# Performance work log

Measured on AMD Instinct MI355X. Metric: run time of the kernel, lower is better.

The kernel has to match this reference:

```python
import jax, jax.numpy as jnp
import numpy as np

N, M, F, NBR = 100000, 12, 64, 64
EPS = 1e-5


def setup_inputs() -> dict:
    key = jax.random.key(0)
    ks = jax.random.split(key, 6)
    atom_in_fea = jax.random.normal(ks[0], (N, F), dtype=jnp.float32)
    nbr_fea = jax.random.normal(ks[1], (N, M, NBR), dtype=jnp.float32)
    bond_weights = jax.random.uniform(ks[2], (N, M), dtype=jnp.float32)
    nbr_fea_idx = jax.random.randint(ks[3], (N, M), 0, N)
    W = jax.random.normal(ks[4], (2 * F, 2 * F + NBR), dtype=jnp.float32) * 0.05
    b = jnp.zeros((2 * F,), dtype=jnp.float32)
    gamma1 = jnp.ones((2 * F,), dtype=jnp.float32)
    beta1 = jnp.zeros((2 * F,), dtype=jnp.float32)
    gamma2 = jnp.ones((F,), dtype=jnp.float32)
    beta2 = jnp.zeros((F,), dtype=jnp.float32)
    return dict(atom_in_fea=atom_in_fea, nbr_fea=nbr_fea, bond_weights=bond_weights,
                nbr_fea_idx=nbr_fea_idx, W=W, b=b, gamma1=gamma1, beta1=beta1,
                gamma2=gamma2, beta2=beta2)


def _batchnorm(x, gamma, beta):
    # training-mode BN over axis 0 with biased variance (torch BatchNorm1d)
    mean = x.mean(axis=0)
    var = ((x - mean) ** 2).mean(axis=0)
    return (x - mean) * jax.lax.rsqrt(var + EPS) * gamma + beta


def reference(atom_in_fea, nbr_fea, bond_weights, nbr_fea_idx, W, b,
              gamma1, beta1, gamma2, beta2):
    n, m = nbr_fea_idx.shape
    f = atom_in_fea.shape[1]
    atom_nbr_fea = atom_in_fea[nbr_fea_idx]                      # (N, M, F) gather
    self_fea = jnp.broadcast_to(atom_in_fea[:, None, :], (n, m, f))
    total = jnp.concatenate([self_fea, atom_nbr_fea, nbr_fea], axis=2)  # (N, M, 2F+NBR)
    gated = jnp.einsum('nmk,ok->nmo', total, W) + b              # (N, M, 2F)
    gated = _batchnorm(gated.reshape(-1, 2 * f), gamma1, beta1).reshape(n, m, 2 * f)
    nbr_filter = jax.nn.sigmoid(gated[..., :f]) * bond_weights[..., None]
    nbr_core = jax.nn.softplus(gated[..., f:]) * bond_weights[..., None]
    nbr_sumed = jnp.sum(nbr_filter * nbr_core, axis=1)           # (N, F)
    nbr_sumed = _batchnorm(nbr_sumed, gamma2, beta2)
    return jax.nn.softplus(atom_in_fea + nbr_sumed)
```

## Files before the change

kernel.cpp:

```cpp
#include <hip/hip_runtime.h>
#include <hip/hip_bf16.h>

typedef unsigned short ushort_t;
typedef __attribute__((ext_vector_type(8))) short bf16x8;
typedef __attribute__((ext_vector_type(4))) float f32x4;

#define NATOM 100000
#define NM    12
#define FD    64
#define KD    192
#define OD    128
#define NGRP  6250
#define ROWS1 1200000.0f
#define EPSBN 1e-5f


__device__ __forceinline__ float bf2f(ushort_t u) {
    unsigned int x = ((unsigned int)u) << 16;
    float f; __builtin_memcpy(&f, &x, 4); return f;
}
__device__ __forceinline__ ushort_t f2b(float f) {
    unsigned int x; __builtin_memcpy(&x, &f, 4);
    x += 0x7FFFu + ((x >> 16) & 1u);
    return (ushort_t)(x >> 16);
}

template<int DT>
__device__ __forceinline__ float ld1(const void* p, long i) {
    if constexpr (DT == 1) return bf2f(((const ushort_t*)p)[i]);
    else                   return ((const float*)p)[i];
}
template<int DT>
__device__ __forceinline__ void st1(void* p, long i, float v) {
    if constexpr (DT == 1) ((ushort_t*)p)[i] = f2b(v);
    else                   ((float*)p)[i] = v;
}
template<int DT>
__device__ __forceinline__ bf16x8 ld8(const void* p, long i) {
    if constexpr (DT == 1) {
        return *(const bf16x8*)((const ushort_t*)p + i);
    } else {
        const float4* f = (const float4*)((const float*)p + i);
        float4 a = f[0], b = f[1];
        bf16x8 r;
        r[0] = (short)f2b(a.x); r[1] = (short)f2b(a.y);
        r[2] = (short)f2b(a.z); r[3] = (short)f2b(a.w);
        r[4] = (short)f2b(b.x); r[5] = (short)f2b(b.y);
        r[6] = (short)f2b(b.z); r[7] = (short)f2b(b.w);
        return r;
    }
}

__global__ void k0_flag(const unsigned int* __restrict__ g1w, int* __restrict__ flag) {
    if (threadIdx.x == 0 && blockIdx.x == 0)
        *flag = (g1w[0] == 0x3F800000u) ? 0 : 1;
}

template<int DT>
__device__ __forceinline__ void stage_W(bf16x8* Wlds, const void* Wg, int tid) {
    for (int c = tid; c < 3072; c += 256) {
        int g = c >> 6, l = c & 63;
        int t = g / 6, s = g % 6;
        int row = t * 16 + (l & 15);
        int col = s * 32 + (l >> 4) * 8;
        Wlds[c] = ld8<DT>(Wg, row * KD + col);
    }
}

template<int DT>
__global__ __launch_bounds__(256) void k1_stats(
    const void* __restrict__ atomg, const void* __restrict__ nbrg,
    const int* __restrict__ idxg, const void* __restrict__ Wg,
    const int* __restrict__ flag, float* __restrict__ s1sum, float* __restrict__ s1sq)
{
    if (*flag != DT) return;
    __shared__ __align__(16) bf16x8 Wlds[3072];
    const int tid = threadIdx.x;
    const int w = tid >> 6, lane = tid & 63, la = lane & 15, q = lane >> 4;

    stage_W<DT>(Wlds, Wg, tid);
    __syncthreads();

    float sum[8], sq[8];
#pragma unroll
    for (int t = 0; t < 8; ++t) { sum[t] = 0.f; sq[t] = 0.f; }

    for (int grp = blockIdx.x; grp < NGRP; grp += gridDim.x) {
        const int n0 = grp << 4;
        const long selfo = (long)(n0 + la) * FD + q * 8;
        for (int it = 0; it < 3; ++it) {
            const int m = it * 4 + w;
            const int nb = idxg[(n0 + la) * NM + m];

            bf16x8 af[6];
            af[0] = ld8<DT>(atomg, selfo);
            af[1] = ld8<DT>(atomg, selfo + 32);
            af[2] = ld8<DT>(atomg, (long)nb * FD + q * 8);
            af[3] = ld8<DT>(atomg, (long)nb * FD + q * 8 + 32);
            af[4] = ld8<DT>(nbrg, ((long)(n0 + la) * NM + m) * FD + q * 8);
            af[5] = ld8<DT>(nbrg, ((long)(n0 + la) * NM + m) * FD + q * 8 + 32);

            f32x4 acc[8];
#pragma unroll
            for (int t = 0; t < 8; ++t) acc[t] = (f32x4){0.f, 0.f, 0.f, 0.f};
#pragma unroll
            for (int s = 0; s < 6; ++s) {
#pragma unroll
                for (int t = 0; t < 8; ++t) {
                    bf16x8 bfr = Wlds[(t * 6 + s) * 64 + lane];
                    acc[t] = __builtin_amdgcn_mfma_f32_16x16x32_bf16(af[s], bfr, acc[t], 0, 0, 0);
                }
            }
#pragma unroll
            for (int t = 0; t < 8; ++t)
#pragma unroll
                for (int r = 0; r < 4; ++r) {
                    float v = acc[t][r];
                    sum[t] += v; sq[t] += v * v;
                }
        }
    }

    const int rep = blockIdx.x & 7;
#pragma unroll
    for (int t = 0; t < 8; ++t) {
        float s = sum[t], z = sq[t];
        s += __shfl_xor(s, 16); s += __shfl_xor(s, 32);
        z += __shfl_xor(z, 16); z += __shfl_xor(z, 32);
        if (lane < 16) {
            atomicAdd(&s1sum[rep * OD + t * 16 + lane], s);
            atomicAdd(&s1sq [rep * OD + t * 16 + lane], z);
        }
    }
}

template<int DT>
__global__ __launch_bounds__(256) void k2_main(
    const void* __restrict__ atomg, const void* __restrict__ nbrg,
    const void* __restrict__ bwg, const int* __restrict__ idxg,
    const void* __restrict__ Wg,
    const void* __restrict__ g1p, const void* __restrict__ b1p,
    const float* __restrict__ s1sum, const float* __restrict__ s1sq,
    const int* __restrict__ flag,
    void* __restrict__ nsum, float* __restrict__ s2sum, float* __restrict__ s2sq)
{
    if (*flag != DT) return;
    __shared__ __align__(16) bf16x8 Wlds[3072];
    __shared__ float pred[4][16][64];
    const int tid = threadIdx.x;
    const int w = tid >> 6, lane = tid & 63, la = lane & 15, q = lane >> 4;

    stage_W<DT>(Wlds, Wg, tid);

    float scale[8], shift[8];
#pragma unroll
    for (int t = 0; t < 8; ++t) {
        int o = t * 16 + la;
        float sm = 0.f, sv = 0.f;
#pragma unroll
        for (int r = 0; r < 8; ++r) { sm += s1sum[r * OD + o]; sv += s1sq[r * OD + o]; }
        float mean = sm / ROWS1;
        float var  = sv / ROWS1 - mean * mean;
        float inv  = 1.0f / sqrtf(var + EPSBN);
        float ga   = ld1<DT>(g1p, o) * inv;
        scale[t] = ga;
        shift[t] = ld1<DT>(b1p, o) - mean * ga;
    }
    __syncthreads();

    float bsum = 0.f, bsq = 0.f;

    for (int grp = blockIdx.x; grp < NGRP; grp += gridDim.x) {
        const int n0 = grp << 4;
        const long selfo = (long)(n0 + la) * FD + q * 8;
        float psum[4][4];
#pragma unroll
        for (int t = 0; t < 4; ++t)
#pragma unroll
            for (int r = 0; r < 4; ++r) psum[t][r] = 0.f;

        for (int it = 0; it < 3; ++it) {
            const int m = it * 4 + w;
            const int nb = idxg[(n0 + la) * NM + m];

            bf16x8 af[6];
            af[0] = ld8<DT>(atomg, selfo);
            af[1] = ld8<DT>(atomg, selfo + 32);
            af[2] = ld8<DT>(atomg, (long)nb * FD + q * 8);
            af[3] = ld8<DT>(atomg, (long)nb * FD + q * 8 + 32);
            af[4] = ld8<DT>(nbrg, ((long)(n0 + la) * NM + m) * FD + q * 8);
            af[5] = ld8<DT>(nbrg, ((long)(n0 + la) * NM + m) * FD + q * 8 + 32);

            f32x4 acc[8];
#pragma unroll
            for (int t = 0; t < 8; ++t) acc[t] = (f32x4){0.f, 0.f, 0.f, 0.f};
#pragma unroll
            for (int s = 0; s < 6; ++s) {
#pragma unroll
                for (int t = 0; t < 8; ++t) {
                    bf16x8 bfr = Wlds[(t * 6 + s) * 64 + lane];
                    acc[t] = __builtin_amdgcn_mfma_f32_16x16x32_bf16(af[s], bfr, acc[t], 0, 0, 0);
                }
            }
#pragma unroll
            for (int r = 0; r < 4; ++r) {
                float bwv = ld1<DT>(bwg, (long)(n0 + q * 4 + r) * NM + m);
                float b2 = bwv * bwv;
#pragma unroll
                for (int t = 0; t < 4; ++t) {
                    float y1 = acc[t][r]     * scale[t]     + shift[t];
                    float y2 = acc[t + 4][r] * scale[t + 4] + shift[t + 4];
                    float sg = 1.0f / (1.0f + __expf(-y1));
                    float ax = fabsf(y2);
                    float sp = fmaxf(y2, 0.0f) + __logf(1.0f + __expf(-ax));
                    psum[t][r] += sg * sp * b2;
                }
            }
        }

#pragma unroll
        for (int t = 0; t < 4; ++t)
#pragma unroll
            for (int r = 0; r < 4; ++r)
                pred[w][q * 4 + r][t * 16 + la] = psum[t][r];
        __syncthreads();
        for (int e = tid; e < 1024; e += 256) {
            int a = e >> 6, c = e & 63;
            float v = pred[0][a][c] + pred[1][a][c] + pred[2][a][c] + pred[3][a][c];
            float vr;
            if constexpr (DT == 1) {
                ushort_t h = f2b(v);
                ((ushort_t*)nsum)[(long)(n0 + a) * FD + c] = h;
                vr = bf2f(h);
            } else {
                ((float*)nsum)[(long)(n0 + a) * FD + c] = v;
                vr = v;
            }
            bsum += vr; bsq += vr * vr;
        }
        __syncthreads();
    }

    const int rep = blockIdx.x & 7;
    atomicAdd(&s2sum[rep * FD + (tid & 63)], bsum);
    atomicAdd(&s2sq [rep * FD + (tid & 63)], bsq);
}

template<int DT>
__global__ __launch_bounds__(256) void k3_final(
    const void* __restrict__ atomg, void* __restrict__ nsum_out,
    const float* __restrict__ s2sum, const float* __restrict__ s2sq,
    const void* __restrict__ g2p, const void* __restrict__ b2p,
    const int* __restrict__ flag)
{
    if (*flag != DT) return;
    const int tid = blockIdx.x * 256 + threadIdx.x;
    const int c = tid & 63;
    float sm = 0.f, sv = 0.f;
#pragma unroll
    for (int r = 0; r < 8; ++r) { sm += s2sum[r * FD + c]; sv += s2sq[r * FD + c]; }
    float mean = sm / 100000.0f;
    float var  = sv / 100000.0f - mean * mean;
    float inv  = 1.0f / sqrtf(var + EPSBN);
    float ga   = ld1<DT>(g2p, c) * inv;
    float sh   = ld1<DT>(b2p, c) - mean * ga;
    float v = ld1<DT>(nsum_out, tid) * ga + sh + ld1<DT>(atomg, tid);
    float ax = fabsf(v);
    float sp = fmaxf(v, 0.0f) + __logf(1.0f + __expf(-ax));
    st1<DT>(nsum_out, tid, sp);
}

extern "C" void kernel_launch(void* const* d_in, const int* in_sizes, int n_in,
                              void* d_out, int out_size, void* d_ws, size_t ws_size,
                              hipStream_t stream) {
    const void* atomg = d_in[0];
    const void* nbrg  = d_in[1];
    const void* bwg   = d_in[2];
    const int*  idxg  = (const int*)d_in[3];
    const void* Wg    = d_in[4];
    const void* g1p   = d_in[6];
    const void* b1p   = d_in[7];
    const void* g2p   = d_in[8];
    const void* b2p   = d_in[9];

    float* wsf   = (float*)d_ws;
    float* s1sum = wsf;
    float* s1sq  = wsf + 1024;
    float* s2sum = wsf + 2048;
    float* s2sq  = wsf + 2560;
    int*   flag  = (int*)(wsf + 4000);

    hipMemsetAsync(d_ws, 0, 16384, stream);

    k0_flag<<<1, 64, 0, stream>>>((const unsigned int*)g1p, flag);

    k1_stats<0><<<768, 256, 0, stream>>>(atomg, nbrg, idxg, Wg, flag, s1sum, s1sq);
    k1_stats<1><<<768, 256, 0, stream>>>(atomg, nbrg, idxg, Wg, flag, s1sum, s1sq);

    k2_main<0><<<512, 256, 0, stream>>>(atomg, nbrg, bwg, idxg, Wg, g1p, b1p,
                                        s1sum, s1sq, flag, d_out, s2sum, s2sq);
    k2_main<1><<<512, 256, 0, stream>>>(atomg, nbrg, bwg, idxg, Wg, g1p, b1p,
                                        s1sum, s1sq, flag, d_out, s2sum, s2sq);

    k3_final<0><<<(NATOM * FD) / 256, 256, 0, stream>>>(atomg, d_out, s2sum, s2sq,
                                                        g2p, b2p, flag);
    k3_final<1><<<(NATOM * FD) / 256, 256, 0, stream>>>(atomg, d_out, s2sum, s2sq,
                                                        g2p, b2p, flag);
}
```

Before: 968.0 us.

## Assign whole atom groups per wavefront with prefetched neighbor loads and no LDS reduction

Each wavefront now owns a full 16-atom group and loops over all 12 neighbors, instead of the four waves of a block splitting the neighbors. Self features are loaded once per group, and the next neighbor's gather is issued before the current MFMA block to overlap memory latency. In k2, the cross-wave LDS reduction and both __syncthreads per group go away because each wave writes its output directly and reduces the BN2 statistics with shuffles. Occupancy hints and a larger k2 grid are added; the prefetch registers could raise register pressure.

```diff
diff --git a/kernel.cpp b/kernel.cpp
--- a/kernel.cpp
+++ b/kernel.cpp
@@ -68,7 +68,20 @@
 }
 
 template<int DT>
-__global__ __launch_bounds__(256) void k1_stats(
+__device__ __forceinline__ void load_m(bf16x8& nb0, bf16x8& nb1, bf16x8& nf0, bf16x8& nf1,
+                                       const void* atomg, const void* nbrg,
+                                       const int* idxg, int n0, int la, int q, int m) {
+    const int nb = idxg[(n0 + la) * NM + m];
+    const long o1 = (long)nb * FD + q * 8;
+    nb0 = ld8<DT>(atomg, o1);
+    nb1 = ld8<DT>(atomg, o1 + 32);
+    const long o2 = ((long)(n0 + la) * NM + m) * FD + q * 8;
+    nf0 = ld8<DT>(nbrg, o2);
+    nf1 = ld8<DT>(nbrg, o2 + 32);
+}
+
+template<int DT>
+__global__ __launch_bounds__(256, 3) void k1_stats(
     const void* __restrict__ atomg, const void* __restrict__ nbrg,
     const int* __restrict__ idxg, const void* __restrict__ Wg,
     const int* __restrict__ flag, float* __restrict__ s1sum, float* __restrict__ s1sq)
@@ -85,32 +98,31 @@
 #pragma unroll
     for (int t = 0; t < 8; ++t) { sum[t] = 0.f; sq[t] = 0.f; }
 
-    for (int grp = blockIdx.x; grp < NGRP; grp += gridDim.x) {
-        const int n0 = grp << 4;
-        const long selfo = (long)(n0 + la) * FD + q * 8;
-        for (int it = 0; it < 3; ++it) {
-            const int m = it * 4 + w;
-            const int nb = idxg[(n0 + la) * NM + m];
-
-            bf16x8 af[6];
-            af[0] = ld8<DT>(atomg, selfo);
-            af[1] = ld8<DT>(atomg, selfo + 32);
-            af[2] = ld8<DT>(atomg, (long)nb * FD + q * 8);
-            af[3] = ld8<DT>(atomg, (long)nb * FD + q * 8 + 32);
-            af[4] = ld8<DT>(nbrg, ((long)(n0 + la) * NM + m) * FD + q * 8);
-            af[5] = ld8<DT>(nbrg, ((long)(n0 + la) * NM + m) * FD + q * 8 + 32);
+    for (int task = blockIdx.x * 4 + w; task < NGRP; task += gridDim.x * 4) {
+        const int n0 = task << 4;
+        const long so = (long)(n0 + la) * FD + q * 8;
+        const bf16x8 self0 = ld8<DT>(atomg, so);
+        const bf16x8 self1 = ld8<DT>(atomg, so + 32);
+
+        bf16x8 cnb0, cnb1, cnf0, cnf1;
+        load_m<DT>(cnb0, cnb1, cnf0, cnf1, atomg, nbrg, idxg, n0, la, q, 0);
+
+        for (int m = 0; m < NM; ++m) {
+            bf16x8 nnb0, nnb1, nnf0, nnf1;
+            const int mn = (m < NM - 1) ? m + 1 : m;
+            load_m<DT>(nnb0, nnb1, nnf0, nnf1, atomg, nbrg, idxg, n0, la, q, mn);
 
             f32x4 acc[8];
 #pragma unroll
             for (int t = 0; t < 8; ++t) acc[t] = (f32x4){0.f, 0.f, 0.f, 0.f};
-#pragma unroll
-            for (int s = 0; s < 6; ++s) {
-#pragma unroll
-                for (int t = 0; t < 8; ++t) {
-                    bf16x8 bfr = Wlds[(t * 6 + s) * 64 + lane];
-                    acc[t] = __builtin_amdgcn_mfma_f32_16x16x32_bf16(af[s], bfr, acc[t], 0, 0, 0);
-                }
-            }
+            const bf16x8 af[6] = {self0, self1, cnb0, cnb1, cnf0, cnf1};
+#pragma unroll
+            for (int s = 0; s < 6; ++s)
+#pragma unroll
+                for (int t = 0; t < 8; ++t)
+                    acc[t] = __builtin_amdgcn_mfma_f32_16x16x32_bf16(
+                        af[s], Wlds[(t * 6 + s) * 64 + lane], acc[t], 0, 0, 0);
+
 #pragma unroll
             for (int t = 0; t < 8; ++t)
 #pragma unroll
@@ -118,6 +130,7 @@
                     float v = acc[t][r];
                     sum[t] += v; sq[t] += v * v;
                 }
+            cnb0 = nnb0; cnb1 = nnb1; cnf0 = nnf0; cnf1 = nnf1;
         }
     }
 
@@ -135,7 +148,7 @@
 }
 
 template<int DT>
-__global__ __launch_bounds__(256) void k2_main(
+__global__ __launch_bounds__(256, 3) void k2_main(
     const void* __restrict__ atomg, const void* __restrict__ nbrg,
     const void* __restrict__ bwg, const int* __restrict__ idxg,
     const void* __restrict__ Wg,
@@ -146,7 +159,6 @@
 {
     if (*flag != DT) return;
     __shared__ __align__(16) bf16x8 Wlds[3072];
-    __shared__ float pred[4][16][64];
     const int tid = threadIdx.x;
     const int w = tid >> 6, lane = tid & 63, la = lane & 15, q = lane >> 4;
 
@@ -168,40 +180,41 @@
     }
     __syncthreads();
 
-    float bsum = 0.f, bsq = 0.f;
-
-    for (int grp = blockIdx.x; grp < NGRP; grp += gridDim.x) {
-        const int n0 = grp << 4;
-        const long selfo = (long)(n0 + la) * FD + q * 8;
+    float bsum[4], bsq[4];
+#pragma unroll
+    for (int t = 0; t < 4; ++t) { bsum[t] = 0.f; bsq[t] = 0.f; }
+
+    for (int task = blockIdx.x * 4 + w; task < NGRP; task += gridDim.x * 4) {
+        const int n0 = task << 4;
+        const long so = (long)(n0 + la) * FD + q * 8;
+        const bf16x8 self0 = ld8<DT>(atomg, so);
+        const bf16x8 self1 = ld8<DT>(atomg, so + 32);
+
         float psum[4][4];
 #pragma unroll
         for (int t = 0; t < 4; ++t)
 #pragma unroll
             for (int r = 0; r < 4; ++r) psum[t][r] = 0.f;
 
-        for (int it = 0; it < 3; ++it) {
-            const int m = it * 4 + w;
-            const int nb = idxg[(n0 + la) * NM + m];
-
-            bf16x8 af[6];
-            af[0] = ld8<DT>(atomg, selfo);
-            af[1] = ld8<DT>(atomg, selfo + 32);
-            af[2] = ld8<DT>(atomg, (long)nb * FD + q * 8);
-            af[3] = ld8<DT>(atomg, (long)nb * FD + q * 8 + 32);
-            af[4] = ld8<DT>(nbrg, ((long)(n0 + la) * NM + m) * FD + q * 8);
-            af[5] = ld8<DT>(nbrg, ((long)(n0 + la) * NM + m) * FD + q * 8 + 32);
+        bf16x8 cnb0, cnb1, cnf0, cnf1;
+        load_m<DT>(cnb0, cnb1, cnf0, cnf1, atomg, nbrg, idxg, n0, la, q, 0);
+
+        for (int m = 0; m < NM; ++m) {
+            bf16x8 nnb0, nnb1, nnf0, nnf1;
+            const int mn = (m < NM - 1) ? m + 1 : m;
+            load_m<DT>(nnb0, nnb1, nnf0, nnf1, atomg, nbrg, idxg, n0, la, q, mn);
 
             f32x4 acc[8];
 #pragma unroll
             for (int t = 0; t < 8; ++t) acc[t] = (f32x4){0.f, 0.f, 0.f, 0.f};
-#pragma unroll
-            for (int s = 0; s < 6; ++s) {
-#pragma unroll
-                for (int t = 0; t < 8; ++t) {
-                    bf16x8 bfr = Wlds[(t * 6 + s) * 64 + lane];
-                    acc[t] = __builtin_amdgcn_mfma_f32_16x16x32_bf16(af[s], bfr, acc[t], 0, 0, 0);
-                }
-            }
+            const bf16x8 af[6] = {self0, self1, cnb0, cnb1, cnf0, cnf1};
+#pragma unroll
+            for (int s = 0; s < 6; ++s)
+#pragma unroll
+                for (int t = 0; t < 8; ++t)
+                    acc[t] = __builtin_amdgcn_mfma_f32_16x16x32_bf16(
+                        af[s], Wlds[(t * 6 + s) * 64 + lane], acc[t], 0, 0, 0);
+
 #pragma unroll
             for (int r = 0; r < 4; ++r) {
                 float bwv = ld1<DT>(bwg, (long)(n0 + q * 4 + r) * NM + m);
@@ -216,34 +229,38 @@
                     psum[t][r] += sg * sp * b2;
                 }
             }
+            cnb0 = nnb0; cnb1 = nnb1; cnf0 = nnf0; cnf1 = nnf1;
         }
 
 #pragma unroll
-        for (int t = 0; t < 4; ++t)
-#pragma unroll
-            for (int r = 0; r < 4; ++r)
-                pred[w][q * 4 + r][t * 16 + la] = psum[t][r];
-        __syncthreads();
-        for (int e = tid; e < 1024; e += 256) {
-            int a = e >> 6, c = e & 63;
-            float v = pred[0][a][c] + pred[1][a][c] + pred[2][a][c] + pred[3][a][c];
-            float vr;
-            if constexpr (DT == 1) {
-                ushort_t h = f2b(v);
-                ((ushort_t*)nsum)[(long)(n0 + a) * FD + c] = h;
-                vr = bf2f(h);
-            } else {
-                ((float*)nsum)[(long)(n0 + a) * FD + c] = v;
-                vr = v;
+        for (int r = 0; r < 4; ++r)
+#pragma unroll
+            for (int t = 0; t < 4; ++t) {
+                float v = psum[t][r];
+                float vr;
+                if constexpr (DT == 1) {
+                    ushort_t h = f2b(v);
+                    ((ushort_t*)nsum)[(long)(n0 + q * 4 + r) * FD + t * 16 + la] = h;
+                    vr = bf2f(h);
+                } else {
+                    ((float*)nsum)[(long)(n0 + q * 4 + r) * FD + t * 16 + la] = v;
+                    vr = v;
+                }
+                bsum[t] += vr; bsq[t] += vr * vr;
             }
-            bsum += vr; bsq += vr * vr;
+    }
+
+    const int rep = blockIdx.x & 7;
+#pragma unroll
+    for (int t = 0; t < 4; ++t) {
+        float s = bsum[t], z = bsq[t];
+        s += __shfl_xor(s, 16); s += __shfl_xor(s, 32);
+        z += __shfl_xor(z, 16); z += __shfl_xor(z, 32);
+        if (lane < 16) {
+            atomicAdd(&s2sum[rep * FD + t * 16 + lane], s);
+            atomicAdd(&s2sq [rep * FD + t * 16 + lane], z);
         }
-        __syncthreads();
-    }
-
-    const int rep = blockIdx.x & 7;
-    atomicAdd(&s2sum[rep * FD + (tid & 63)], bsum);
-    atomicAdd(&s2sq [rep * FD + (tid & 63)], bsq);
+    }
 }
 
 template<int DT>
@@ -297,9 +314,9 @@
     k1_stats<0><<<768, 256, 0, stream>>>(atomg, nbrg, idxg, Wg, flag, s1sum, s1sq);
     k1_stats<1><<<768, 256, 0, stream>>>(atomg, nbrg, idxg, Wg, flag, s1sum, s1sq);
 
-    k2_main<0><<<512, 256, 0, stream>>>(atomg, nbrg, bwg, idxg, Wg, g1p, b1p,
+    k2_main<0><<<768, 256, 0, stream>>>(atomg, nbrg, bwg, idxg, Wg, g1p, b1p,
                                         s1sum, s1sq, flag, d_out, s2sum, s2sq);
-    k2_main<1><<<512, 256, 0, stream>>>(atomg, nbrg, bwg, idxg, Wg, g1p, b1p,
+    k2_main<1><<<768, 256, 0, stream>>>(atomg, nbrg, bwg, idxg, Wg, g1p, b1p,
                                         s1sum, s1sq, flag, d_out, s2sum, s2sq);
 
     k3_final<0><<<(NATOM * FD) / 256, 256, 0, stream>>>(atomg, d_out, s2sum, s2sq,
```

New measurement: 1.557 ms. 1.61x slower.
